# Optimization experiments

Measured on AMD Instinct MI355X. Metric: run time of the kernel, lower is better.

Reference implementation:

```python
import jax, jax.numpy as jnp
import numpy as np

N_NODES = 50000
N_EDGES = 800000
D_IN = 128
D_HID = 128
D_OUT = 1
N_GRAPHS = 64


def gcn_conv(x, edge_index, W, b):
    """PyG GCNConv: add self-loops, symmetric deg^-1/2 normalization, xW, scatter-add, +bias."""
    n = x.shape[0]
    loops = jnp.arange(n, dtype=edge_index.dtype)
    row = jnp.concatenate([edge_index[0], loops])  # source nodes
    col = jnp.concatenate([edge_index[1], loops])  # destination nodes
    deg = jax.ops.segment_sum(jnp.ones_like(col, dtype=x.dtype), col, num_segments=n)
    dinv = jax.lax.rsqrt(jnp.maximum(deg, 1.0))  # deg >= 1 due to self-loops
    norm = dinv[row] * dinv[col]                 # [E+N]
    h = x @ W                                    # [N, d_out] dense GEMM first (cheaper than per-edge)
    msgs = h[row] * norm[:, None]                # gather + scale, [E+N, d_out]
    out = jax.ops.segment_sum(msgs, col, num_segments=n)  # scatter-add
    return out + b


def setup_inputs() -> dict:
    key = jax.random.key(0)
    ks = jax.random.split(key, 12)
    x = jax.random.normal(ks[0], (N_NODES, D_IN), dtype=jnp.float32)
    edge_index = jax.random.randint(ks[1], (2, N_EDGES), 0, N_NODES, dtype=jnp.int64)
    batch = jnp.sort(jax.random.randint(ks[2], (N_NODES,), 0, N_GRAPHS, dtype=jnp.int64))
    s_in = 1.0 / np.sqrt(D_IN)
    s_hid = 1.0 / np.sqrt(D_HID)
    W0 = jax.random.uniform(ks[3], (D_IN, D_HID), jnp.float32, -s_in, s_in)
    b0 = jnp.zeros((D_HID,), jnp.float32)
    W1 = jax.random.uniform(ks[4], (D_HID, D_HID), jnp.float32, -s_hid, s_hid)
    b1 = jnp.zeros((D_HID,), jnp.float32)
    W2 = jax.random.uniform(ks[5], (D_HID, D_HID), jnp.float32, -s_hid, s_hid)
    b2 = jnp.zeros((D_HID,), jnp.float32)
    fc_w = jax.random.uniform(ks[6], (D_HID, D_OUT), jnp.float32, -s_hid, s_hid)
    fc_b = jax.random.uniform(ks[7], (D_OUT,), jnp.float32, -s_hid, s_hid)
    return {"x": x, "edge_index": edge_index, "batch": batch,
            "W0": W0, "b0": b0, "W1": W1, "b1": b1, "W2": W2, "b2": b2,
            "fc_w": fc_w, "fc_b": fc_b}


def reference(x, edge_index, batch, W0, b0, W1, b1, W2, b2, fc_w, fc_b):
    h = x
    for W, b in ((W0, b0), (W1, b1), (W2, b2)):  # 3 GCN layers (structural, not data loop)
        h = jax.nn.relu(gcn_conv(h, edge_index, W, b))
    # global_mean_pool over graph ids
    sums = jax.ops.segment_sum(h, batch, num_segments=N_GRAPHS)          # [G, d]
    counts = jax.ops.segment_sum(jnp.ones((h.shape[0],), h.dtype), batch, num_segments=N_GRAPHS)
    pooled = sums / jnp.maximum(counts, 1.0)[:, None]
    return pooled @ fc_w + fc_b  # [G, 1]
```

## Files before the change

### kernel.cpp

```cpp
#include <hip/hip_runtime.h>

#define DH 128
#define NGRAPH 64

static __device__ __forceinline__ float4 f4fma(float a, float4 b, float4 c) {
  c.x = fmaf(a, b.x, c.x); c.y = fmaf(a, b.y, c.y);
  c.z = fmaf(a, b.z, c.z); c.w = fmaf(a, b.w, c.w);
  return c;
}

__global__ void count_deg_k(const int* __restrict__ col, int* __restrict__ deg, int e) {
  int i = blockIdx.x * blockDim.x + threadIdx.x;
  if (i < e) atomicAdd(&deg[col[i]], 1);
}

__global__ __launch_bounds__(512) void scan1_k(const int* __restrict__ deg, int* __restrict__ incl,
                                               int* __restrict__ blksum, int n) {
  __shared__ int s[512];
  int t = threadIdx.x;
  int i = blockIdx.x * 512 + t;
  int v = (i < n) ? deg[i] : 0;
  s[t] = v;
  __syncthreads();
  #pragma unroll
  for (int off = 1; off < 512; off <<= 1) {
    int x = (t >= off) ? s[t - off] : 0;
    __syncthreads();
    s[t] += x;
    __syncthreads();
  }
  if (i < n) incl[i] = s[t];
  if (t == 511) blksum[blockIdx.x] = s[511];
}

__global__ __launch_bounds__(128) void scan2_k(int* __restrict__ blksum, int nb) {
  __shared__ int s[128];
  int t = threadIdx.x;
  int v = (t < nb) ? blksum[t] : 0;
  s[t] = v;
  __syncthreads();
  #pragma unroll
  for (int off = 1; off < 128; off <<= 1) {
    int x = (t >= off) ? s[t - off] : 0;
    __syncthreads();
    s[t] += x;
    __syncthreads();
  }
  if (t < nb) blksum[t] = s[t] - v;
}

__global__ __launch_bounds__(512) void scan3_k(const int* __restrict__ deg, int* __restrict__ ptr,
                                               const int* __restrict__ blkoff, int* __restrict__ cursor,
                                               float* __restrict__ dinv, int n, int e) {
  int i = blockIdx.x * 512 + threadIdx.x;
  if (i < n) {
    int cnt = deg[i];
    int excl = ptr[i] - cnt + blkoff[i >> 9];
    ptr[i] = excl;
    cursor[i] = excl;
    dinv[i] = rsqrtf((float)(cnt + 1));
  }
  if (i == 0) ptr[n] = e;
}

__global__ void scatter_k(const int* __restrict__ row, const int* __restrict__ col,
                          int* __restrict__ cursor, int* __restrict__ csr_src, int e) {
  int i = blockIdx.x * blockDim.x + threadIdx.x;
  if (i < e) {
    int c = col[i];
    int pos = atomicAdd(&cursor[c], 1);
    csr_src[pos] = row[i];
  }
}

__global__ __launch_bounds__(256, 3) void gemm_k(const float* __restrict__ A, const float* __restrict__ W,
                                                 const float* __restrict__ dinv,
                                                 float* __restrict__ C, int M) {
  __shared__ float xs[64][64];
  __shared__ float ws[64][128];
  const int tid = threadIdx.x;
  const int tx = tid & 31;
  const int ty = tid >> 5;
  const int m_base = blockIdx.x * 64;

  float4 acc[8];
  #pragma unroll
  for (int i = 0; i < 8; i++) acc[i] = make_float4(0.f, 0.f, 0.f, 0.f);

  for (int kc = 0; kc < 128; kc += 64) {
    const float4* Wg = (const float4*)(W + kc * DH);
    float4* wsv = (float4*)ws;
    #pragma unroll
    for (int i = 0; i < 8; i++) wsv[tid + 256 * i] = Wg[tid + 256 * i];
    #pragma unroll
    for (int i = 0; i < 4; i++) {
      int f = tid + 256 * i;
      int m = f >> 4;
      int k4 = (f & 15) << 2;
      int r = m_base + m;
      if (r >= M) r = M - 1;
      *(float4*)&xs[m][k4] = *(const float4*)(A + (size_t)r * DH + kc + k4);
    }
    __syncthreads();
    #pragma unroll 4
    for (int k = 0; k < 64; k += 4) {
      float4 wb0 = *(const float4*)&ws[k + 0][tx * 4];
      float4 wb1 = *(const float4*)&ws[k + 1][tx * 4];
      float4 wb2 = *(const float4*)&ws[k + 2][tx * 4];
      float4 wb3 = *(const float4*)&ws[k + 3][tx * 4];
      #pragma unroll
      for (int i = 0; i < 8; i++) {
        float4 xa = *(const float4*)&xs[ty * 8 + i][k];
        acc[i] = f4fma(xa.x, wb0, acc[i]);
        acc[i] = f4fma(xa.y, wb1, acc[i]);
        acc[i] = f4fma(xa.z, wb2, acc[i]);
        acc[i] = f4fma(xa.w, wb3, acc[i]);
      }
    }
    __syncthreads();
  }
  #pragma unroll
  for (int i = 0; i < 8; i++) {
    int r = m_base + ty * 8 + i;
    int rc = (r < M) ? r : (M - 1);
    float dsc = dinv[rc];
    acc[i].x *= dsc; acc[i].y *= dsc; acc[i].z *= dsc; acc[i].w *= dsc;
    *(float4*)(C + (size_t)r * DH + tx * 4) = acc[i];
  }
}

__global__ __launch_bounds__(256) void aggregate_k(const float* __restrict__ hs, const float* __restrict__ dinv,
                                                   const int* __restrict__ ptr, const int* __restrict__ csr_src,
                                                   const float* __restrict__ bias, float* __restrict__ out, int n) {
  int wave = threadIdx.x >> 6;
  int lane = threadIdx.x & 63;
  int node = blockIdx.x * 4 + wave;
  if (node >= n) return;
  const float2* h2 = (const float2*)hs;
  float di = dinv[node];
  int e0 = ptr[node], e1 = ptr[node + 1];
  float2 a0 = h2[(size_t)node * 64 + lane];
  float2 a1 = make_float2(0.f, 0.f);
  float2 a2 = make_float2(0.f, 0.f);
  float2 a3 = make_float2(0.f, 0.f);
  int e = e0;
  for (; e + 4 <= e1; e += 4) {
    int s0 = csr_src[e + 0];
    int s1 = csr_src[e + 1];
    int s2 = csr_src[e + 2];
    int s3 = csr_src[e + 3];
    float2 v0 = h2[(size_t)s0 * 64 + lane];
    float2 v1 = h2[(size_t)s1 * 64 + lane];
    float2 v2 = h2[(size_t)s2 * 64 + lane];
    float2 v3 = h2[(size_t)s3 * 64 + lane];
    a0.x += v0.x; a0.y += v0.y;
    a1.x += v1.x; a1.y += v1.y;
    a2.x += v2.x; a2.y += v2.y;
    a3.x += v3.x; a3.y += v3.y;
  }
  for (; e < e1; ++e) {
    int s = csr_src[e];
    float2 v = h2[(size_t)s * 64 + lane];
    a0.x += v.x; a0.y += v.y;
  }
  float sx = (a0.x + a1.x) + (a2.x + a3.x);
  float sy = (a0.y + a1.y) + (a2.y + a3.y);
  float2 b = *(const float2*)(bias + lane * 2);
  sx = fmaxf(fmaf(sx, di, b.x), 0.f);
  sy = fmaxf(fmaf(sy, di, b.y), 0.f);
  ((float2*)out)[(size_t)node * 64 + lane] = make_float2(sx, sy);
}

__global__ void count_batch_k(const int* __restrict__ batch, int* __restrict__ gcnt, int n) {
  int i = blockIdx.x * blockDim.x + threadIdx.x;
  bool active = (i < n);
  int g = active ? batch[i] : 0;
  unsigned long long act = __ballot(active);
  if (!active) return;
  int first = __ffsll((long long)act) - 1;
  int g0 = __shfl(g, first);
  bool uni = __all(g == g0);
  int lane = threadIdx.x & 63;
  if (uni) {
    if (lane == first) atomicAdd(&gcnt[g], (int)__popcll(act));
  } else {
    atomicAdd(&gcnt[g], 1);
  }
}

#define POOL_CHUNK 50
__global__ __launch_bounds__(128) void pool_partial_k(const float* __restrict__ h, const int* __restrict__ batch,
                                                      float* __restrict__ pooled, int n) {
  int n0 = blockIdx.x * POOL_CHUNK;
  if (n0 >= n) return;
  int n1 = n0 + POOL_CHUNK; if (n1 > n) n1 = n;
  int d = threadIdx.x;
  float acc = 0.f;
  int gp = batch[n0];
  for (int i = n0; i < n1; ++i) {
    int g = batch[i];
    if (g != gp) { atomicAdd(&pooled[(size_t)gp * DH + d], acc); acc = 0.f; gp = g; }
    acc += h[(size_t)i * DH + d];
  }
  atomicAdd(&pooled[(size_t)gp * DH + d], acc);
}

__global__ void final_k(const float* __restrict__ pooled, const int* __restrict__ gcnt,
                        const float* __restrict__ fcw, const float* __restrict__ fcb,
                        float* __restrict__ out) {
  int g = threadIdx.x;
  if (g >= NGRAPH) return;
  float c = fmaxf((float)gcnt[g], 1.f);
  float s = 0.f;
  #pragma unroll 4
  for (int d = 0; d < DH; ++d) s = fmaf(pooled[(size_t)g * DH + d] / c, fcw[d], s);
  out[g] = s + fcb[0];
}

extern "C" void kernel_launch(void* const* d_in, const int* in_sizes, int n_in,
                              void* d_out, int out_size, void* d_ws, size_t ws_size,
                              hipStream_t stream) {
  const float* x    = (const float*)d_in[0];
  const int*   ei   = (const int*)d_in[1];
  const int*   batch= (const int*)d_in[2];
  const float* W0   = (const float*)d_in[3];
  const float* b0   = (const float*)d_in[4];
  const float* W1   = (const float*)d_in[5];
  const float* b1   = (const float*)d_in[6];
  const float* W2   = (const float*)d_in[7];
  const float* b2   = (const float*)d_in[8];
  const float* fcw  = (const float*)d_in[9];
  const float* fcb  = (const float*)d_in[10];
  float* out = (float*)d_out;

  const int N = in_sizes[0] / DH;
  const int E = in_sizes[1] / 2;
  const int* row = ei;
  const int* col = ei + E;
  const int MPAD = ((N + 63) / 64) * 64;

  char* ws = (char*)d_ws;
  size_t off = 0;
  auto carve = [&](size_t bytes) -> char* {
    char* p = ws + off;
    off = (off + bytes + 255) & ~(size_t)255;
    return p;
  };
  float* bufA    = (float*)carve((size_t)MPAD * DH * 4);
  float* bufB    = (float*)carve((size_t)MPAD * DH * 4);
  int*   deg     = (int*)carve((size_t)N * 4);
  float* dinv    = (float*)carve((size_t)N * 4);
  int*   csr_ptr = (int*)carve((size_t)(N + 1) * 4);
  int*   cursor  = (int*)carve((size_t)N * 4);
  int*   csr_src = (int*)carve((size_t)E * 4);
  int*   blksum  = (int*)carve(128 * 4);
  int*   gcnt    = (int*)carve(NGRAPH * 4);
  float* pooled  = (float*)carve((size_t)NGRAPH * DH * 4);
  (void)ws_size; (void)n_in; (void)out_size;

  const int nb256N = (N + 255) / 256;
  const int nb256E = (E + 255) / 256;
  const int nbScan = (N + 511) / 512;

  hipMemsetAsync(deg, 0, (size_t)N * 4, stream);
  hipMemsetAsync(gcnt, 0, NGRAPH * 4, stream);
  hipMemsetAsync(pooled, 0, (size_t)NGRAPH * DH * 4, stream);

  count_deg_k<<<nb256E, 256, 0, stream>>>(col, deg, E);
  count_batch_k<<<nb256N, 256, 0, stream>>>(batch, gcnt, N);

  scan1_k<<<nbScan, 512, 0, stream>>>(deg, csr_ptr, blksum, N);
  scan2_k<<<1, 128, 0, stream>>>(blksum, nbScan);
  scan3_k<<<nbScan, 512, 0, stream>>>(deg, csr_ptr, blksum, cursor, dinv, N, E);
  scatter_k<<<nb256E, 256, 0, stream>>>(row, col, cursor, csr_src, E);

  const int gemmBlocks = MPAD / 64;
  const int aggBlocks = (N + 3) / 4;

  gemm_k<<<gemmBlocks, 256, 0, stream>>>(x, W0, dinv, bufA, N);
  aggregate_k<<<aggBlocks, 256, 0, stream>>>(bufA, dinv, csr_ptr, csr_src, b0, bufB, N);
  gemm_k<<<gemmBlocks, 256, 0, stream>>>(bufB, W1, dinv, bufA, N);
  aggregate_k<<<aggBlocks, 256, 0, stream>>>(bufA, dinv, csr_ptr, csr_src, b1, bufB, N);
  gemm_k<<<gemmBlocks, 256, 0, stream>>>(bufB, W2, dinv, bufA, N);
  aggregate_k<<<aggBlocks, 256, 0, stream>>>(bufA, dinv, csr_ptr, csr_src, b2, bufB, N);

  const int poolBlocks = (N + POOL_CHUNK - 1) / POOL_CHUNK;
  pool_partial_k<<<poolBlocks, 128, 0, stream>>>(bufB, batch, pooled, N);
  final_k<<<1, 64, 0, stream>>>(pooled, gcnt, fcw, fcb, out);
}
```

Before: 502.8 us.

## Build CSR via two-pass source-sorted scatter, direct-load GEMM A, unroll aggregation by 8

Edges are first bucketed by source into a temporary buffer and then scattered by destination, so each destination's neighbor list ends up sorted by source id. This aims to improve locality of the gathers in aggregation. The GEMM drops the shared-memory staging of A and reads rows directly from global memory with a smaller W tile, and the aggregation loop is unrolled to 8 independent accumulators for more memory-level parallelism. In exchange the build does an extra degree count, scan and scatter pass, and the uncached direct A loads may raise global traffic in the GEMM.

```diff
diff --git a/kernel.cpp b/kernel.cpp
--- a/kernel.cpp
+++ b/kernel.cpp
@@ -9,14 +9,22 @@
   return c;
 }
 
-__global__ void count_deg_k(const int* __restrict__ col, int* __restrict__ deg, int e) {
+__global__ void count_both_k(const int* __restrict__ row, const int* __restrict__ col,
+                             int* __restrict__ deg_dst, int* __restrict__ deg_src, int e) {
   int i = blockIdx.x * blockDim.x + threadIdx.x;
-  if (i < e) atomicAdd(&deg[col[i]], 1);
-}
-
-__global__ __launch_bounds__(512) void scan1_k(const int* __restrict__ deg, int* __restrict__ incl,
-                                               int* __restrict__ blksum, int n) {
+  if (i < e) {
+    atomicAdd(&deg_dst[col[i]], 1);
+    atomicAdd(&deg_src[row[i]], 1);
+  }
+}
+
+__global__ __launch_bounds__(512) void scan1_pair_k(const int* __restrict__ deg_dst, const int* __restrict__ deg_src,
+                                                    int* __restrict__ incl_dst, int* __restrict__ incl_src,
+                                                    int* __restrict__ blksum, int n) {
   __shared__ int s[512];
+  int which = blockIdx.y;
+  const int* deg = which ? deg_src : deg_dst;
+  int* incl = which ? incl_src : incl_dst;
   int t = threadIdx.x;
   int i = blockIdx.x * 512 + t;
   int v = (i < n) ? deg[i] : 0;
@@ -30,13 +38,14 @@
     __syncthreads();
   }
   if (i < n) incl[i] = s[t];
-  if (t == 511) blksum[blockIdx.x] = s[511];
-}
-
-__global__ __launch_bounds__(128) void scan2_k(int* __restrict__ blksum, int nb) {
+  if (t == 511) blksum[which * 128 + blockIdx.x] = s[511];
+}
+
+__global__ __launch_bounds__(128) void scan2_pair_k(int* __restrict__ blksum, int nb) {
   __shared__ int s[128];
+  int* b = blksum + blockIdx.x * 128;
   int t = threadIdx.x;
-  int v = (t < nb) ? blksum[t] : 0;
+  int v = (t < nb) ? b[t] : 0;
   s[t] = v;
   __syncthreads();
   #pragma unroll
@@ -46,71 +55,91 @@
     s[t] += x;
     __syncthreads();
   }
-  if (t < nb) blksum[t] = s[t] - v;
-}
-
-__global__ __launch_bounds__(512) void scan3_k(const int* __restrict__ deg, int* __restrict__ ptr,
-                                               const int* __restrict__ blkoff, int* __restrict__ cursor,
-                                               float* __restrict__ dinv, int n, int e) {
+  if (t < nb) b[t] = s[t] - v;
+}
+
+__global__ __launch_bounds__(512) void scan3_pair_k(const int* __restrict__ deg_dst, const int* __restrict__ deg_src,
+                                                    int* __restrict__ csr_ptr, int* __restrict__ cur_dst,
+                                                    int* __restrict__ cur_src, const int* __restrict__ blkoff,
+                                                    float* __restrict__ dinv, int n, int e) {
+  int which = blockIdx.y;
   int i = blockIdx.x * 512 + threadIdx.x;
-  if (i < n) {
-    int cnt = deg[i];
-    int excl = ptr[i] - cnt + blkoff[i >> 9];
-    ptr[i] = excl;
-    cursor[i] = excl;
-    dinv[i] = rsqrtf((float)(cnt + 1));
-  }
-  if (i == 0) ptr[n] = e;
-}
-
-__global__ void scatter_k(const int* __restrict__ row, const int* __restrict__ col,
-                          int* __restrict__ cursor, int* __restrict__ csr_src, int e) {
+  if (which == 0) {
+    if (i < n) {
+      int cnt = deg_dst[i];
+      int excl = csr_ptr[i] - cnt + blkoff[i >> 9];
+      csr_ptr[i] = excl;
+      cur_dst[i] = excl;
+      dinv[i] = rsqrtf((float)(cnt + 1));
+    }
+    if (i == 0) csr_ptr[n] = e;
+  } else {
+    if (i < n) {
+      int cnt = deg_src[i];
+      int excl = cur_src[i] - cnt + blkoff[128 + (i >> 9)];
+      cur_src[i] = excl;
+    }
+  }
+}
+
+__global__ void scatter_src_k(const int* __restrict__ row, const int* __restrict__ col,
+                              int* __restrict__ cur_src, int2* __restrict__ tmp, int e) {
   int i = blockIdx.x * blockDim.x + threadIdx.x;
   if (i < e) {
-    int c = col[i];
-    int pos = atomicAdd(&cursor[c], 1);
-    csr_src[pos] = row[i];
-  }
-}
-
-__global__ __launch_bounds__(256, 3) void gemm_k(const float* __restrict__ A, const float* __restrict__ W,
-                                                 const float* __restrict__ dinv,
-                                                 float* __restrict__ C, int M) {
-  __shared__ float xs[64][64];
-  __shared__ float ws[64][128];
+    int s = row[i], d = col[i];
+    int p = atomicAdd(&cur_src[s], 1);
+    tmp[p] = make_int2(s, d);
+  }
+}
+
+__global__ void scatter_dst_k(const int2* __restrict__ tmp, int* __restrict__ cur_dst,
+                              int* __restrict__ csr_src, int e) {
+  int i = blockIdx.x * blockDim.x + threadIdx.x;
+  if (i < e) {
+    int2 t = tmp[i];
+    int p = atomicAdd(&cur_dst[t.y], 1);
+    csr_src[p] = t.x;
+  }
+}
+
+__global__ __launch_bounds__(256) void gemm_k(const float* __restrict__ A, const float* __restrict__ W,
+                                              const float* __restrict__ dinv,
+                                              float* __restrict__ C, int M) {
+  __shared__ float ws4[32][128];
   const int tid = threadIdx.x;
   const int tx = tid & 31;
   const int ty = tid >> 5;
   const int m_base = blockIdx.x * 64;
 
+  const float* ar[8];
+  #pragma unroll
+  for (int i = 0; i < 8; i++) {
+    int r = m_base + ty * 8 + i;
+    if (r >= M) r = M - 1;
+    ar[i] = A + (size_t)r * DH;
+  }
+
   float4 acc[8];
   #pragma unroll
   for (int i = 0; i < 8; i++) acc[i] = make_float4(0.f, 0.f, 0.f, 0.f);
 
-  for (int kc = 0; kc < 128; kc += 64) {
+  for (int kc = 0; kc < 128; kc += 32) {
     const float4* Wg = (const float4*)(W + kc * DH);
-    float4* wsv = (float4*)ws;
+    float4* wsv = (float4*)ws4;
+    wsv[tid] = Wg[tid];
+    wsv[tid + 256] = Wg[tid + 256];
+    wsv[tid + 512] = Wg[tid + 512];
+    wsv[tid + 768] = Wg[tid + 768];
+    __syncthreads();
     #pragma unroll
-    for (int i = 0; i < 8; i++) wsv[tid + 256 * i] = Wg[tid + 256 * i];
-    #pragma unroll
-    for (int i = 0; i < 4; i++) {
-      int f = tid + 256 * i;
-      int m = f >> 4;
-      int k4 = (f & 15) << 2;
-      int r = m_base + m;
-      if (r >= M) r = M - 1;
-      *(float4*)&xs[m][k4] = *(const float4*)(A + (size_t)r * DH + kc + k4);
-    }
-    __syncthreads();
-    #pragma unroll 4
-    for (int k = 0; k < 64; k += 4) {
-      float4 wb0 = *(const float4*)&ws[k + 0][tx * 4];
-      float4 wb1 = *(const float4*)&ws[k + 1][tx * 4];
-      float4 wb2 = *(const float4*)&ws[k + 2][tx * 4];
-      float4 wb3 = *(const float4*)&ws[k + 3][tx * 4];
+    for (int k = 0; k < 32; k += 4) {
+      float4 wb0 = *(const float4*)&ws4[k + 0][tx * 4];
+      float4 wb1 = *(const float4*)&ws4[k + 1][tx * 4];
+      float4 wb2 = *(const float4*)&ws4[k + 2][tx * 4];
+      float4 wb3 = *(const float4*)&ws4[k + 3][tx * 4];
       #pragma unroll
       for (int i = 0; i < 8; i++) {
-        float4 xa = *(const float4*)&xs[ty * 8 + i][k];
+        float4 xa = *(const float4*)(ar[i] + kc + k);
         acc[i] = f4fma(xa.x, wb0, acc[i]);
         acc[i] = f4fma(xa.y, wb1, acc[i]);
         acc[i] = f4fma(xa.z, wb2, acc[i]);
@@ -140,15 +169,30 @@
   float di = dinv[node];
   int e0 = ptr[node], e1 = ptr[node + 1];
   float2 a0 = h2[(size_t)node * 64 + lane];
-  float2 a1 = make_float2(0.f, 0.f);
-  float2 a2 = make_float2(0.f, 0.f);
-  float2 a3 = make_float2(0.f, 0.f);
+  float2 a1 = make_float2(0.f, 0.f), a2 = a1, a3 = a1, a4 = a1, a5 = a1, a6 = a1, a7 = a1;
   int e = e0;
+  for (; e + 8 <= e1; e += 8) {
+    int s0 = csr_src[e + 0], s1 = csr_src[e + 1], s2 = csr_src[e + 2], s3 = csr_src[e + 3];
+    int s4 = csr_src[e + 4], s5 = csr_src[e + 5], s6 = csr_src[e + 6], s7 = csr_src[e + 7];
+    float2 v0 = h2[(size_t)s0 * 64 + lane];
+    float2 v1 = h2[(size_t)s1 * 64 + lane];
+    float2 v2 = h2[(size_t)s2 * 64 + lane];
+    float2 v3 = h2[(size_t)s3 * 64 + lane];
+    float2 v4 = h2[(size_t)s4 * 64 + lane];
+    float2 v5 = h2[(size_t)s5 * 64 + lane];
+    float2 v6 = h2[(size_t)s6 * 64 + lane];
+    float2 v7 = h2[(size_t)s7 * 64 + lane];
+    a0.x += v0.x; a0.y += v0.y;
+    a1.x += v1.x; a1.y += v1.y;
+    a2.x += v2.x; a2.y += v2.y;
+    a3.x += v3.x; a3.y += v3.y;
+    a4.x += v4.x; a4.y += v4.y;
+    a5.x += v5.x; a5.y += v5.y;
+    a6.x += v6.x; a6.y += v6.y;
+    a7.x += v7.x; a7.y += v7.y;
+  }
   for (; e + 4 <= e1; e += 4) {
-    int s0 = csr_src[e + 0];
-    int s1 = csr_src[e + 1];
-    int s2 = csr_src[e + 2];
-    int s3 = csr_src[e + 3];
+    int s0 = csr_src[e + 0], s1 = csr_src[e + 1], s2 = csr_src[e + 2], s3 = csr_src[e + 3];
     float2 v0 = h2[(size_t)s0 * 64 + lane];
     float2 v1 = h2[(size_t)s1 * 64 + lane];
     float2 v2 = h2[(size_t)s2 * 64 + lane];
@@ -163,8 +207,8 @@
     float2 v = h2[(size_t)s * 64 + lane];
     a0.x += v.x; a0.y += v.y;
   }
-  float sx = (a0.x + a1.x) + (a2.x + a3.x);
-  float sy = (a0.y + a1.y) + (a2.y + a3.y);
+  float sx = ((a0.x + a1.x) + (a2.x + a3.x)) + ((a4.x + a5.x) + (a6.x + a7.x));
+  float sy = ((a0.y + a1.y) + (a2.y + a3.y)) + ((a4.y + a5.y) + (a6.y + a7.y));
   float2 b = *(const float2*)(bias + lane * 2);
   sx = fmaxf(fmaf(sx, di, b.x), 0.f);
   sy = fmaxf(fmaf(sy, di, b.y), 0.f);
@@ -248,31 +292,37 @@
   };
   float* bufA    = (float*)carve((size_t)MPAD * DH * 4);
   float* bufB    = (float*)carve((size_t)MPAD * DH * 4);
-  int*   deg     = (int*)carve((size_t)N * 4);
+  int*   deg2    = (int*)carve((size_t)2 * N * 4);
   float* dinv    = (float*)carve((size_t)N * 4);
   int*   csr_ptr = (int*)carve((size_t)(N + 1) * 4);
-  int*   cursor  = (int*)carve((size_t)N * 4);
+  int*   cur_dst = (int*)carve((size_t)N * 4);
+  int*   cur_src = (int*)carve((size_t)N * 4);
   int*   csr_src = (int*)carve((size_t)E * 4);
-  int*   blksum  = (int*)carve(128 * 4);
+  int*   blksum  = (int*)carve(256 * 4);
   int*   gcnt    = (int*)carve(NGRAPH * 4);
   float* pooled  = (float*)carve((size_t)NGRAPH * DH * 4);
   (void)ws_size; (void)n_in; (void)out_size;
 
+  int* deg_dst = deg2;
+  int* deg_src = deg2 + N;
+  int2* tmp = (int2*)bufA;
+
   const int nb256N = (N + 255) / 256;
   const int nb256E = (E + 255) / 256;
   const int nbScan = (N + 511) / 512;
 
-  hipMemsetAsync(deg, 0, (size_t)N * 4, stream);
-  hipMemsetAsync(gcnt, 0, NGRAPH * 4, stream);
-  hipMemsetAsync(pooled, 0, (size_t)NGRAPH * DH * 4, stream);
-
-  count_deg_k<<<nb256E, 256, 0, stream>>>(col, deg, E);
+  hipMemsetAsync(deg2, 0, (size_t)2 * N * 4, stream);
+  hipMemsetAsync(gcnt, 0, NGRAPH * 4 + (size_t)NGRAPH * DH * 4, stream);
+
+  count_both_k<<<nb256E, 256, 0, stream>>>(row, col, deg_dst, deg_src, E);
   count_batch_k<<<nb256N, 256, 0, stream>>>(batch, gcnt, N);
 
-  scan1_k<<<nbScan, 512, 0, stream>>>(deg, csr_ptr, blksum, N);
-  scan2_k<<<1, 128, 0, stream>>>(blksum, nbScan);
-  scan3_k<<<nbScan, 512, 0, stream>>>(deg, csr_ptr, blksum, cursor, dinv, N, E);
-  scatter_k<<<nb256E, 256, 0, stream>>>(row, col, cursor, csr_src, E);
+  scan1_pair_k<<<dim3(nbScan, 2), 512, 0, stream>>>(deg_dst, deg_src, csr_ptr, cur_src, blksum, N);
+  scan2_pair_k<<<2, 128, 0, stream>>>(blksum, nbScan);
+  scan3_pair_k<<<dim3(nbScan, 2), 512, 0, stream>>>(deg_dst, deg_src, csr_ptr, cur_dst, cur_src,
+                                                    blksum, dinv, N, E);
+  scatter_src_k<<<nb256E, 256, 0, stream>>>(row, col, cur_src, tmp, E);
+  scatter_dst_k<<<nb256E, 256, 0, stream>>>(tmp, cur_dst, csr_src, E);
 
   const int gemmBlocks = MPAD / 64;
   const int aggBlocks = (N + 3) / 4;
```

Result: slower. 602.2 us (+19.8%).
